# Kernel tuning notes

Measured on AMD Instinct MI355X. Metric: run time of the kernel, lower is better.

## Reference

```python
import jax, jax.numpy as jnp
import numpy as np

M, N, K = 1024, 11008, 4096


def _unpack_i2u(Bp):
    """Unpack 2-bit unsigned weights per decode_i2u_to_i8s interleave.

    Bp: [N, K//4] int8 storage. Within each group of 4 bytes (16 elements),
    output element at position 4*i + j = (byte_j >> (2*i)) & 3.
    Returns [N, K] int8 with values in {0,1,2,3}.
    """
    Bu = jax.lax.bitcast_convert_type(Bp, jnp.uint8)  # [N, K//4]
    n, kc = Bu.shape
    Bg = Bu.reshape(n, kc // 4, 1, 4)                 # [N, G, 1, j]
    shifts = (jnp.arange(4, dtype=jnp.uint8) * jnp.uint8(2)).reshape(1, 1, 4, 1)
    vals = (Bg >> shifts) & jnp.uint8(3)              # [N, G, i, j]
    return vals.reshape(n, kc * 4).astype(jnp.int8)   # [N, K]


def setup_inputs() -> dict:
    key = jax.random.key(0)
    k1, k2 = jax.random.split(key)
    A = jax.random.randint(k1, (M, K), -128, 128, dtype=jnp.int8)
    B = jax.random.randint(k2, (N, K // 4), -128, 128, dtype=jnp.int8)
    return {"A": A, "B": B}


def reference(A, B):
    W = _unpack_i2u(B)  # [N, K] int8
    C = jax.lax.dot_general(
        A, W,
        dimension_numbers=(((1,), (1,)), ((), ())),
        preferred_element_type=jnp.int32,
    )  # [M, N] int32
    return C
```

## Files before the change

kernel.cpp:

```cpp
#include <hip/hip_runtime.h>
#include <stdint.h>


#define MM 1024
#define NN 11008
#define KK 4096
#define MTILES 8
#define NTILES 86
#define NBLOCKS (MTILES * NTILES)
#define STRIDE_A ((size_t)MTILES * 8192)
#define STRIDE_B ((size_t)NTILES * 2048)

using i32x4  = __attribute__((ext_vector_type(4))) int;
using i32x16 = __attribute__((ext_vector_type(16))) int;

__device__ __forceinline__ int pack4(i32x4 v) {
    return (int)(((uint32_t)v[0] & 0xFFu) | (((uint32_t)v[1] & 0xFFu) << 8)
               | (((uint32_t)v[2] & 0xFFu) << 16) | (((uint32_t)v[3] & 0xFFu) << 24));
}

__global__ __launch_bounds__(256) void prep_AB(const int* __restrict__ Asrc,
                                               const int* __restrict__ Bsrc,
                                               uint8_t* __restrict__ A2,
                                               uint8_t* __restrict__ B3) {
    if (blockIdx.x < 1024) {
        const int g = blockIdx.x * 256 + threadIdx.x;
        const int kstep = g >> 12;
        const int rem   = g & 4095;
        const int mtile = rem >> 9;
        const int c     = rem & 511;
        const int row32 = (c >> 7) & 3, kk2 = (c >> 6) & 1;
        const int lane  = c & 63;
        const int row   = mtile * 128 + row32 * 32 + (lane & 31);
        const int kbyte = kstep * 64 + kk2 * 32 + (lane >> 5) * 16;
        const i32x4* s4 = (const i32x4*)(Asrc + (size_t)row * KK + kbyte);
        i32x4 o;
#pragma unroll
        for (int q = 0; q < 4; ++q) o[q] = pack4(s4[q]);
        *(i32x4*)(A2 + (size_t)g * 16) = o;
    } else {
        const int t = (blockIdx.x - 1024) * 256 + threadIdx.x;
        const int n = t >> 6, kstep = t & 63;
        const int ntile = n >> 7, hf = (n >> 6) & 1, ni = (n >> 5) & 1, l31 = n & 31;
        const i32x4* s4 = (const i32x4*)(Bsrc + (size_t)n * (KK / 4) + kstep * 16);
        int w[4];
#pragma unroll
        for (int j = 0; j < 4; ++j) w[j] = pack4(s4[j]);
        uint8_t* base = B3 + ((size_t)kstep * NTILES + ntile) * 2048 + hf * 1024;
        *(int2*)(base + l31 * 16 + ni * 8)        = make_int2(w[0], w[2]);
        *(int2*)(base + (l31 + 32) * 16 + ni * 8) = make_int2(w[1], w[3]);
    }
}

#define GLOAD_LDS16(g, l) __builtin_amdgcn_global_load_lds(                    \
        (const __attribute__((address_space(1))) uint32_t*)(g),                \
        (__attribute__((address_space(3))) uint32_t*)(l), 16, 0, 0)

#define MFMA_I8 __builtin_amdgcn_mfma_i32_32x32x32_i8

#define PSTAGE(T) do {                                                         \
    const uint8_t* at_ = gA + (size_t)(T) * STRIDE_A;                          \
    const uint8_t* bt_ = gB + (size_t)(T) * STRIDE_B;                          \
    uint8_t* l_ = &As[(T) & 3][0];                                             \
    GLOAD_LDS16(at_,        l_);                                               \
    GLOAD_LDS16(at_ + 1024, l_ + 1024);                                        \
    GLOAD_LDS16(at_ + 2048, l_ + 2048);                                        \
    GLOAD_LDS16(at_ + 3072, l_ + 3072);                                        \
    GLOAD_LDS16(at_ + 4096, l_ + 4096);                                        \
    GLOAD_LDS16(at_ + 5120, l_ + 5120);                                        \
    GLOAD_LDS16(at_ + 6144, l_ + 6144);                                        \
    GLOAD_LDS16(at_ + 7168, l_ + 7168);                                        \
    GLOAD_LDS16(bt_,        l_ + 8192);                                        \
    GLOAD_LDS16(bt_ + 1024, l_ + 9216);                                        \
} while (0)

#define COMP(T) do {                                                           \
    const uint8_t* ab_ = &As[(T) & 3][0];                                      \
    i32x4 aA0_ = *(const i32x4*)(ab_ + (wr * 2 + 0) * 2048 + lane * 16);       \
    i32x4 aA1_ = *(const i32x4*)(ab_ + (wr * 2 + 0) * 2048 + 1024 + lane * 16);\
    i32x4 aB0_ = *(const i32x4*)(ab_ + (wr * 2 + 1) * 2048 + lane * 16);       \
    i32x4 aB1_ = *(const i32x4*)(ab_ + (wr * 2 + 1) * 2048 + 1024 + lane * 16);\
    const i32x4 bv_ = *(const i32x4*)(ab_ + 8192 + wc * 1024 + lane * 16);     \
    _Pragma("unroll")                                                          \
    for (int kk2_ = 0; kk2_ < 2; ++kk2_) {                                     \
        const uint32_t q0_ = (uint32_t)bv_[kk2_];                              \
        const uint32_t q1_ = (uint32_t)bv_[2 + kk2_];                          \
        i32x4 b0_, b1_;                                                        \
        _Pragma("unroll")                                                      \
        for (int i_ = 0; i_ < 4; ++i_) {                                       \
            b0_[i_] = (int)((q0_ >> (2 * i_)) & 0x03030303u);                  \
            b1_[i_] = (int)((q1_ >> (2 * i_)) & 0x03030303u);                  \
        }                                                                      \
        const i32x4 am0_ = kk2_ ? aA1_ : aA0_;                                 \
        const i32x4 am1_ = kk2_ ? aB1_ : aB0_;                                 \
        acc[0][0] = MFMA_I8(am0_, b0_, acc[0][0], 0, 0, 0);                    \
        acc[0][1] = MFMA_I8(am0_, b1_, acc[0][1], 0, 0, 0);                    \
        acc[1][0] = MFMA_I8(am1_, b0_, acc[1][0], 0, 0, 0);                    \
        acc[1][1] = MFMA_I8(am1_, b1_, acc[1][1], 0, 0, 0);                    \
    }                                                                          \
} while (0)

#define PWAIT(N) asm volatile("s_waitcnt vmcnt(" #N ")" ::: "memory")

__global__ __launch_bounds__(320, 3) void bitnet_gemm(const uint8_t* __restrict__ A2,
                                                      const uint8_t* __restrict__ B3,
                                                      int* __restrict__ C) {
    const int tid  = threadIdx.x;
    const int lane = tid & 63, wave = tid >> 6;
    const int wr   = (wave >> 1) & 1, wc = wave & 1;
    const int l31  = lane & 31, h = lane >> 5;

    const int bid = blockIdx.x;
    const int l   = (bid & 7) * (NBLOCKS / 8) + (bid >> 3);
    const int bm  = l & 7;
    const int bn  = l >> 3;

    __shared__ __align__(16) uint8_t As[4][10240];

    if (wave == 4) {
        const uint8_t* gA = A2 + (size_t)bm * 8192 + lane * 16;
        const uint8_t* gB = B3 + (size_t)bn * 2048 + lane * 16;

        PSTAGE(0); PSTAGE(1); PSTAGE(2);
        PWAIT(20);
#pragma unroll 1
        for (int t = 0; t < 60; t += 4) {
            __builtin_amdgcn_s_barrier(); PSTAGE(t + 3); PWAIT(20);
            __builtin_amdgcn_s_barrier(); PSTAGE(t + 4); PWAIT(20);
            __builtin_amdgcn_s_barrier(); PSTAGE(t + 5); PWAIT(20);
            __builtin_amdgcn_s_barrier(); PSTAGE(t + 6); PWAIT(20);
        }
        __builtin_amdgcn_s_barrier(); PSTAGE(63); PWAIT(20);
        __builtin_amdgcn_s_barrier(); PWAIT(10);
        __builtin_amdgcn_s_barrier(); PWAIT(0);
        __builtin_amdgcn_s_barrier();
        return;
    }

    i32x16 acc[2][2] = {};

#pragma unroll 1
    for (int t = 0; t < 64; t += 4) {
        __builtin_amdgcn_s_barrier();
        __builtin_amdgcn_sched_barrier(0);
        COMP(t + 0);
        __builtin_amdgcn_s_barrier();
        __builtin_amdgcn_sched_barrier(0);
        COMP(t + 1);
        __builtin_amdgcn_s_barrier();
        __builtin_amdgcn_sched_barrier(0);
        COMP(t + 2);
        __builtin_amdgcn_s_barrier();
        __builtin_amdgcn_sched_barrier(0);
        COMP(t + 3);
    }

    const int brow = bm * 128, bcol = bn * 128;
#pragma unroll
    for (int mi = 0; mi < 2; ++mi)
#pragma unroll
        for (int ni = 0; ni < 2; ++ni) {
            const int colg = bcol + wc * 64 + ni * 32 + l31;
#pragma unroll
            for (int r = 0; r < 16; ++r) {
                const int rowin = (r & 3) + 8 * (r >> 2) + 4 * h;
                const int rowg  = brow + wr * 64 + mi * 32 + rowin;
                C[(size_t)rowg * NN + colg] = acc[mi][ni][r];
            }
        }
}

extern "C" void kernel_launch(void* const* d_in, const int* in_sizes, int n_in,
                              void* d_out, int out_size, void* d_ws, size_t ws_size,
                              hipStream_t stream) {
    const int* A32 = (const int*)d_in[0];
    const int* B32 = (const int*)d_in[1];
    int* C = (int*)d_out;

    uint8_t* A2 = (uint8_t*)d_ws;
    uint8_t* B3 = A2 + (size_t)MM * KK;

    prep_AB<<<dim3(1024 + 2752), dim3(256), 0, stream>>>(A32, B32, A2, B3);
    bitnet_gemm<<<dim3(NBLOCKS), dim3(320), 0, stream>>>(A2, B3, C);
}
```

Before: 63.77 us.

## Deepen LDS ring to five stages and double-buffer fragment reads in registers

Result: slower. 66.59 us (+4.4%).

```diff
diff --git a/kernel.cpp b/kernel.cpp
--- a/kernel.cpp
+++ b/kernel.cpp
@@ -61,7 +61,7 @@
 #define PSTAGE(T) do {                                                         \
     const uint8_t* at_ = gA + (size_t)(T) * STRIDE_A;                          \
     const uint8_t* bt_ = gB + (size_t)(T) * STRIDE_B;                          \
-    uint8_t* l_ = &As[(T) & 3][0];                                             \
+    uint8_t* l_ = &As[(T) % 5][0];                                             \
     GLOAD_LDS16(at_,        l_);                                               \
     GLOAD_LDS16(at_ + 1024, l_ + 1024);                                        \
     GLOAD_LDS16(at_ + 2048, l_ + 2048);                                        \
@@ -74,33 +74,36 @@
     GLOAD_LDS16(bt_ + 1024, l_ + 9216);                                        \
 } while (0)
 
-#define COMP(T) do {                                                           \
-    const uint8_t* ab_ = &As[(T) & 3][0];                                      \
-    i32x4 aA0_ = *(const i32x4*)(ab_ + (wr * 2 + 0) * 2048 + lane * 16);       \
-    i32x4 aA1_ = *(const i32x4*)(ab_ + (wr * 2 + 0) * 2048 + 1024 + lane * 16);\
-    i32x4 aB0_ = *(const i32x4*)(ab_ + (wr * 2 + 1) * 2048 + lane * 16);       \
-    i32x4 aB1_ = *(const i32x4*)(ab_ + (wr * 2 + 1) * 2048 + 1024 + lane * 16);\
-    const i32x4 bv_ = *(const i32x4*)(ab_ + 8192 + wc * 1024 + lane * 16);     \
+#define PWAIT(N) asm volatile("s_waitcnt vmcnt(" #N ")" ::: "memory")
+
+#define READF(BUF, T) do {                                                     \
+    const uint8_t* ab_ = &As[(T) % 5][0];                                      \
+    BUF##_a00 = *(const i32x4*)(ab_ + (wr * 2 + 0) * 2048 + lane * 16);        \
+    BUF##_a01 = *(const i32x4*)(ab_ + (wr * 2 + 0) * 2048 + 1024 + lane * 16); \
+    BUF##_a10 = *(const i32x4*)(ab_ + (wr * 2 + 1) * 2048 + lane * 16);        \
+    BUF##_a11 = *(const i32x4*)(ab_ + (wr * 2 + 1) * 2048 + 1024 + lane * 16); \
+    BUF##_bv  = *(const i32x4*)(ab_ + 8192 + wc * 1024 + lane * 16);           \
+} while (0)
+
+#define COMPR(BUF) do {                                                        \
     _Pragma("unroll")                                                          \
     for (int kk2_ = 0; kk2_ < 2; ++kk2_) {                                     \
-        const uint32_t q0_ = (uint32_t)bv_[kk2_];                              \
-        const uint32_t q1_ = (uint32_t)bv_[2 + kk2_];                          \
+        const uint32_t q0_ = (uint32_t)BUF##_bv[kk2_];                         \
+        const uint32_t q1_ = (uint32_t)BUF##_bv[2 + kk2_];                     \
         i32x4 b0_, b1_;                                                        \
         _Pragma("unroll")                                                      \
         for (int i_ = 0; i_ < 4; ++i_) {                                       \
             b0_[i_] = (int)((q0_ >> (2 * i_)) & 0x03030303u);                  \
             b1_[i_] = (int)((q1_ >> (2 * i_)) & 0x03030303u);                  \
         }                                                                      \
-        const i32x4 am0_ = kk2_ ? aA1_ : aA0_;                                 \
-        const i32x4 am1_ = kk2_ ? aB1_ : aB0_;                                 \
+        const i32x4 am0_ = kk2_ ? BUF##_a01 : BUF##_a00;                       \
+        const i32x4 am1_ = kk2_ ? BUF##_a11 : BUF##_a10;                       \
         acc[0][0] = MFMA_I8(am0_, b0_, acc[0][0], 0, 0, 0);                    \
         acc[0][1] = MFMA_I8(am0_, b1_, acc[0][1], 0, 0, 0);                    \
         acc[1][0] = MFMA_I8(am1_, b0_, acc[1][0], 0, 0, 0);                    \
         acc[1][1] = MFMA_I8(am1_, b1_, acc[1][1], 0, 0, 0);                    \
     }                                                                          \
 } while (0)
-
-#define PWAIT(N) asm volatile("s_waitcnt vmcnt(" #N ")" ::: "memory")
 
 __global__ __launch_bounds__(320, 3) void bitnet_gemm(const uint8_t* __restrict__ A2,
                                                       const uint8_t* __restrict__ B3,
@@ -115,44 +118,44 @@
     const int bm  = l & 7;
     const int bn  = l >> 3;
 
-    __shared__ __align__(16) uint8_t As[4][10240];
+    __shared__ __align__(16) uint8_t As[5][10240];
 
     if (wave == 4) {
         const uint8_t* gA = A2 + (size_t)bm * 8192 + lane * 16;
         const uint8_t* gB = B3 + (size_t)bn * 2048 + lane * 16;
 
-        PSTAGE(0); PSTAGE(1); PSTAGE(2);
+        PSTAGE(0); PSTAGE(1); PSTAGE(2); PSTAGE(3);
         PWAIT(20);
+        __builtin_amdgcn_s_barrier();
 #pragma unroll 1
         for (int t = 0; t < 60; t += 4) {
-            __builtin_amdgcn_s_barrier(); PSTAGE(t + 3); PWAIT(20);
-            __builtin_amdgcn_s_barrier(); PSTAGE(t + 4); PWAIT(20);
-            __builtin_amdgcn_s_barrier(); PSTAGE(t + 5); PWAIT(20);
-            __builtin_amdgcn_s_barrier(); PSTAGE(t + 6); PWAIT(20);
+            PSTAGE(t + 4); PWAIT(20); __builtin_amdgcn_s_barrier();
+            PSTAGE(t + 5); PWAIT(20); __builtin_amdgcn_s_barrier();
+            PSTAGE(t + 6); PWAIT(20); __builtin_amdgcn_s_barrier();
+            PSTAGE(t + 7); PWAIT(20); __builtin_amdgcn_s_barrier();
         }
-        __builtin_amdgcn_s_barrier(); PSTAGE(63); PWAIT(20);
-        __builtin_amdgcn_s_barrier(); PWAIT(10);
-        __builtin_amdgcn_s_barrier(); PWAIT(0);
+        PWAIT(10); __builtin_amdgcn_s_barrier();
+        PWAIT(0);  __builtin_amdgcn_s_barrier();
+        __builtin_amdgcn_s_barrier();
         __builtin_amdgcn_s_barrier();
         return;
     }
 
     i32x16 acc[2][2] = {};
+    i32x4 b0_a00, b0_a01, b0_a10, b0_a11, b0_bv;
+    i32x4 b1_a00, b1_a01, b1_a10, b1_a11, b1_bv;
+
+    __builtin_amdgcn_s_barrier();
+    READF(b0, 0);
 
 #pragma unroll 1
-    for (int t = 0; t < 64; t += 4) {
+    for (int t = 0; t < 64; t += 2) {
         __builtin_amdgcn_s_barrier();
-        __builtin_amdgcn_sched_barrier(0);
-        COMP(t + 0);
+        if (t + 1 < 64) READF(b1, t + 1);
+        COMPR(b0);
         __builtin_amdgcn_s_barrier();
-        __builtin_amdgcn_sched_barrier(0);
-        COMP(t + 1);
-        __builtin_amdgcn_s_barrier();
-        __builtin_amdgcn_sched_barrier(0);
-        COMP(t + 2);
-        __builtin_amdgcn_s_barrier();
-        __builtin_amdgcn_sched_barrier(0);
-        COMP(t + 3);
+        if (t + 2 < 64) READF(b0, t + 2);
+        COMPR(b1);
     }
 
     const int brow = bm * 128, bcol = bn * 128;
```

## Convert GEMM to persistent blocks pulling tiles from an atomic counter

Applied to the files above, without the earlier changes.

After: 87.30 us. 1.37x slower.

```diff
diff --git a/kernel.cpp b/kernel.cpp
--- a/kernel.cpp
+++ b/kernel.cpp
@@ -7,7 +7,8 @@
 #define KK 4096
 #define MTILES 8
 #define NTILES 86
-#define NBLOCKS (MTILES * NTILES)
+#define NTILES_TOT (MTILES * NTILES)
+#define NPERS 768
 #define STRIDE_A ((size_t)MTILES * 8192)
 #define STRIDE_B ((size_t)NTILES * 2048)
 
@@ -101,73 +102,70 @@
 } while (0)
 
 #define PWAIT(N) asm volatile("s_waitcnt vmcnt(" #N ")" ::: "memory")
+#define BAR()    __builtin_amdgcn_s_barrier()
 
 __global__ __launch_bounds__(320, 3) void bitnet_gemm(const uint8_t* __restrict__ A2,
                                                       const uint8_t* __restrict__ B3,
-                                                      int* __restrict__ C) {
+                                                      int* __restrict__ C,
+                                                      int* __restrict__ counter) {
     const int tid  = threadIdx.x;
     const int lane = tid & 63, wave = tid >> 6;
     const int wr   = (wave >> 1) & 1, wc = wave & 1;
     const int l31  = lane & 31, h = lane >> 5;
 
-    const int bid = blockIdx.x;
-    const int l   = (bid & 7) * (NBLOCKS / 8) + (bid >> 3);
-    const int bm  = l & 7;
-    const int bn  = l >> 3;
+    __shared__ __align__(16) uint8_t As[4][10240];
+    __shared__ int tile_s;
 
-    __shared__ __align__(16) uint8_t As[4][10240];
+    for (;;) {
+        if (tid == 0) tile_s = atomicAdd(counter, 1);
+        __syncthreads();
+        const int tl = tile_s;
+        if (tl >= NTILES_TOT) return;
 
-    if (wave == 4) {
-        const uint8_t* gA = A2 + (size_t)bm * 8192 + lane * 16;
-        const uint8_t* gB = B3 + (size_t)bn * 2048 + lane * 16;
+        const int bm = tl & 7;
+        const int bn = tl >> 3;
 
-        PSTAGE(0); PSTAGE(1); PSTAGE(2);
-        PWAIT(20);
+        if (wave == 4) {
+            const uint8_t* gA = A2 + (size_t)bm * 8192 + lane * 16;
+            const uint8_t* gB = B3 + (size_t)bn * 2048 + lane * 16;
+
+            PSTAGE(0); PSTAGE(1); PSTAGE(2);
+            PWAIT(20);
 #pragma unroll 1
-        for (int t = 0; t < 60; t += 4) {
-            __builtin_amdgcn_s_barrier(); PSTAGE(t + 3); PWAIT(20);
-            __builtin_amdgcn_s_barrier(); PSTAGE(t + 4); PWAIT(20);
-            __builtin_amdgcn_s_barrier(); PSTAGE(t + 5); PWAIT(20);
-            __builtin_amdgcn_s_barrier(); PSTAGE(t + 6); PWAIT(20);
+            for (int t = 0; t < 60; t += 4) {
+                BAR(); PSTAGE(t + 3); PWAIT(20);
+                BAR(); PSTAGE(t + 4); PWAIT(20);
+                BAR(); PSTAGE(t + 5); PWAIT(20);
+                BAR(); PSTAGE(t + 6); PWAIT(20);
+            }
+            BAR(); PSTAGE(63); PWAIT(20);
+            BAR(); PWAIT(10);
+            BAR(); PWAIT(0);
+            BAR();
+        } else {
+            i32x16 acc[2][2] = {};
+#pragma unroll 1
+            for (int t = 0; t < 64; t += 4) {
+                BAR(); __builtin_amdgcn_sched_barrier(0); COMP(t + 0);
+                BAR(); __builtin_amdgcn_sched_barrier(0); COMP(t + 1);
+                BAR(); __builtin_amdgcn_sched_barrier(0); COMP(t + 2);
+                BAR(); __builtin_amdgcn_sched_barrier(0); COMP(t + 3);
+            }
+            const int brow = bm * 128, bcol = bn * 128;
+#pragma unroll
+            for (int mi = 0; mi < 2; ++mi)
+#pragma unroll
+                for (int ni = 0; ni < 2; ++ni) {
+                    const int colg = bcol + wc * 64 + ni * 32 + l31;
+#pragma unroll
+                    for (int r = 0; r < 16; ++r) {
+                        const int rowin = (r & 3) + 8 * (r >> 2) + 4 * h;
+                        const int rowg  = brow + wr * 64 + mi * 32 + rowin;
+                        C[(size_t)rowg * NN + colg] = acc[mi][ni][r];
+                    }
+                }
         }
-        __builtin_amdgcn_s_barrier(); PSTAGE(63); PWAIT(20);
-        __builtin_amdgcn_s_barrier(); PWAIT(10);
-        __builtin_amdgcn_s_barrier(); PWAIT(0);
-        __builtin_amdgcn_s_barrier();
-        return;
     }
-
-    i32x16 acc[2][2] = {};
-
-#pragma unroll 1
-    for (int t = 0; t < 64; t += 4) {
-        __builtin_amdgcn_s_barrier();
-        __builtin_amdgcn_sched_barrier(0);
-        COMP(t + 0);
-        __builtin_amdgcn_s_barrier();
-        __builtin_amdgcn_sched_barrier(0);
-        COMP(t + 1);
-        __builtin_amdgcn_s_barrier();
-        __builtin_amdgcn_sched_barrier(0);
-        COMP(t + 2);
-        __builtin_amdgcn_s_barrier();
-        __builtin_amdgcn_sched_barrier(0);
-        COMP(t + 3);
-    }
-
-    const int brow = bm * 128, bcol = bn * 128;
-#pragma unroll
-    for (int mi = 0; mi < 2; ++mi)
-#pragma unroll
-        for (int ni = 0; ni < 2; ++ni) {
-            const int colg = bcol + wc * 64 + ni * 32 + l31;
-#pragma unroll
-            for (int r = 0; r < 16; ++r) {
-                const int rowin = (r & 3) + 8 * (r >> 2) + 4 * h;
-                const int rowg  = brow + wr * 64 + mi * 32 + rowin;
-                C[(size_t)rowg * NN + colg] = acc[mi][ni][r];
-            }
-        }
 }
 
 extern "C" void kernel_launch(void* const* d_in, const int* in_sizes, int n_in,
@@ -179,7 +177,9 @@
 
     uint8_t* A2 = (uint8_t*)d_ws;
     uint8_t* B3 = A2 + (size_t)MM * KK;
+    int* counter = (int*)(B3 + (size_t)NN * (KK / 4));
 
+    hipMemsetAsync(counter, 0, sizeof(int), stream);
     prep_AB<<<dim3(1024 + 2752), dim3(256), 0, stream>>>(A32, B32, A2, B3);
-    bitnet_gemm<<<dim3(NBLOCKS), dim3(320), 0, stream>>>(A2, B3, C);
+    bitnet_gemm<<<dim3(NPERS), dim3(320), 0, stream>>>(A2, B3, C, counter);
 }
```
